# Optimization experiments

Measured on AMD Instinct MI355X. Metric: run time of the kernel, lower is better.

The kernel has to match this reference:

```python
import jax, jax.numpy as jnp
import numpy as np

N_NODES = 50000
N_EDGES = 1600000
HIDDEN = 1024
NUM_CLASSES = 64


def setup_inputs() -> dict:
    key = jax.random.key(0)
    k1, k2, k3 = jax.random.split(key, 3)
    x = jax.random.normal(k1, (N_NODES, HIDDEN), dtype=jnp.float32)
    edge_index = jax.random.randint(k2, (2, N_EDGES), 0, N_NODES, dtype=jnp.int64)
    # Glorot-style init for the GCNConv linear weight, zero bias (PyG defaults)
    W = jax.random.normal(k3, (HIDDEN, NUM_CLASSES), dtype=jnp.float32) / np.sqrt(HIDDEN)
    b = jnp.zeros((NUM_CLASSES,), dtype=jnp.float32)
    return {"x": x, "edge_index": edge_index, "W": W, "b": b}


def reference(x, edge_index, W, b):
    # GCNConv: add self-loops, symmetric deg^{-1/2} normalization,
    # linear transform, gather-scale-scatter aggregation, bias, then softmax.
    n = x.shape[0]
    loops = jnp.arange(n, dtype=edge_index.dtype)
    src = jnp.concatenate([edge_index[0], loops])  # [E+N]
    dst = jnp.concatenate([edge_index[1], loops])  # [E+N]

    ones = jnp.ones(dst.shape[0], dtype=x.dtype)
    deg = jax.ops.segment_sum(ones, dst, num_segments=n)  # in-degree incl. self-loop
    deg_inv_sqrt = jnp.where(deg > 0, jax.lax.rsqrt(deg), 0.0)
    norm = deg_inv_sqrt[src] * deg_inv_sqrt[dst]  # [E+N]

    h = x @ W  # [N, C] dense GEMM (transform before propagate)
    msgs = h[src] * norm[:, None]  # gather + scale
    out = jax.ops.segment_sum(msgs, dst, num_segments=n) + b  # scatter-add
    return jax.nn.softmax(out, axis=1)
```

## Files before the change

kernel.cpp:

```cpp
#include <hip/hip_runtime.h>
#include <hip/hip_bf16.h>
#include <hip/hip_fp16.h>
#include <math.h>

#define HIDDEN 1024
#define NCLS 64
#define NB2 784
#define BCAP2 2560
#define CHUNK 4096
#define SMEM_BYTES 33280

typedef __attribute__((ext_vector_type(8))) short short8;
typedef __attribute__((ext_vector_type(4))) float f32x4;
typedef __attribute__((ext_vector_type(8))) _Float16 half8;

__device__ __forceinline__ short f2bf(float f) {
    __hip_bfloat16 b = __float2bfloat16(f);
    return __builtin_bit_cast(short, b);
}
__device__ __forceinline__ float bf2f(short s) {
    unsigned u = ((unsigned)(unsigned short)s) << 16;
    return __builtin_bit_cast(float, u);
}

__device__ __forceinline__ void async_copy16(void* lds, const void* g) {
    __builtin_amdgcn_global_load_lds(
        (const __attribute__((address_space(1))) unsigned int*)g,
        (__attribute__((address_space(3))) unsigned int*)lds, 16, 0, 0);
}

__global__ void wprep_kernel(const float* __restrict__ W,
                             short* __restrict__ wt_hi, short* __restrict__ wt_lo) {
    int idx = blockIdx.x * 256 + threadIdx.x;
    int c = idx >> 10;
    int k = idx & 1023;
    float f = W[(size_t)k * NCLS + c];
    short hb = f2bf(f);
    wt_hi[idx] = hb;
    wt_lo[idx] = f2bf(f - bf2f(hb));
}

__device__ void bucket_body(char* smem, const int* __restrict__ ei,
                            unsigned* __restrict__ pairs2, int* __restrict__ bcnt2,
                            int E, int bid) {
    int* hist  = (int*)smem;
    int* offs  = hist + 1024;
    int* cur   = offs + 1024;
    int* gbase = cur + 1024;
    unsigned* stage = (unsigned*)(gbase + 1024);
    int* nz = (int*)(stage + CHUNK);
    int* wsum = nz + 1;

    const int tid = threadIdx.x;
    const int base = bid * CHUNK;
    const int cnt_c = min(CHUNK, E - base);

    if (tid == 0) *nz = 0;
    #pragma unroll
    for (int j = 0; j < 4; ++j) { hist[tid + 256 * j] = 0; cur[tid + 256 * j] = 0; }
    __syncthreads();

    int found = 0;
    for (int j = tid; j < 1024; j += 256) {
        int e = base + j;
        if (e < E) found |= (ei[2 * e + 1] != 0);
    }
    if (found) atomicOr(nz, 1);
    __syncthreads();
    const int is64 = (*nz == 0);

    unsigned pr[16];
    #pragma unroll
    for (int j = 0; j < 16; ++j) {
        int e = base + j * 256 + tid;
        unsigned p = 0xFFFFFFFFu;
        if (e < E) {
            int s = is64 ? ei[2 * e] : ei[e];
            int d = is64 ? ei[2 * (E + e)] : ei[E + e];
            p = (unsigned)s | ((unsigned)d << 16);
            atomicAdd(&hist[d >> 6], 1);
        }
        pr[j] = p;
    }
    __syncthreads();

    const int b0 = 4 * tid;
    int h0 = hist[b0], h1 = hist[b0 + 1], h2 = hist[b0 + 2], h3 = hist[b0 + 3];
    int S = h0 + h1 + h2 + h3;
    int incl = S;
    #pragma unroll
    for (int d = 1; d < 64; d <<= 1) {
        int t2 = __shfl_up(incl, d);
        if ((tid & 63) >= d) incl += t2;
    }
    if ((tid & 63) == 63) wsum[tid >> 6] = incl;
    __syncthreads();
    int pre = 0;
    #pragma unroll
    for (int w = 0; w < 4; ++w)
        if (w < (tid >> 6)) pre += wsum[w];
    int ex = pre + incl - S;
    offs[b0] = ex;
    offs[b0 + 1] = ex + h0;
    offs[b0 + 2] = ex + h0 + h1;
    offs[b0 + 3] = ex + h0 + h1 + h2;
    if (h0 > 0) gbase[b0] = atomicAdd(&bcnt2[b0], h0);
    if (h1 > 0) gbase[b0 + 1] = atomicAdd(&bcnt2[b0 + 1], h1);
    if (h2 > 0) gbase[b0 + 2] = atomicAdd(&bcnt2[b0 + 2], h2);
    if (h3 > 0) gbase[b0 + 3] = atomicAdd(&bcnt2[b0 + 3], h3);
    __syncthreads();

    #pragma unroll
    for (int j = 0; j < 16; ++j) {
        unsigned p = pr[j];
        if (p != 0xFFFFFFFFu) {
            int b = (int)(p >> 22);
            int pos = offs[b] + atomicAdd(&cur[b], 1);
            stage[pos] = p;
        }
    }
    __syncthreads();
    for (int i = tid; i < cnt_c; i += 256) {
        unsigned p = stage[i];
        int b = (int)(p >> 22);
        pairs2[(size_t)b * BCAP2 + gbase[b] + (i - offs[b])] = p;
    }
    __syncthreads();
}

__device__ void gemm_body(char* smem, const float* __restrict__ x,
                          const short* __restrict__ wt_hi, const short* __restrict__ wt_lo,
                          _Float16* __restrict__ h16, int M, int bid) {
    char* As = smem;
    char* Bh = smem + 16 * 1040;
    char* Bl = smem + 24 * 1040;

    const int tid = threadIdx.x;
    const int wave = tid >> 6;
    const int lane = tid & 63;
    const int l15 = lane & 15, l4 = lane >> 4;
    const int row0 = bid * 64;

    const float* agp[4];
    #pragma unroll
    for (int i = 0; i < 4; ++i) {
        int rg = row0 + (wave * 4 + i) * 4 + (lane >> 4);
        if (rg > M - 1) rg = M - 1;
        int g = (lane & 15) ^ (((lane >> 4) & 3) << 2);
        agp[i] = x + (size_t)rg * HIDDEN + g * 4;
    }
    const short* bhp[2];
    const short* blp[2];
    #pragma unroll
    for (int i = 0; i < 2; ++i) {
        int c = (wave * 2 + i) * 8 + (lane >> 3);
        int g = (lane & 7) ^ ((lane >> 3) & 7);
        bhp[i] = wt_hi + (size_t)c * HIDDEN + g * 8;
        blp[i] = wt_lo + (size_t)c * HIDDEN + g * 8;
    }

    f32x4 acc[4];
    #pragma unroll
    for (int nf = 0; nf < 4; ++nf) acc[nf] = (f32x4){0.f, 0.f, 0.f, 0.f};

    const int rt = wave * 16 + l15;
    const int r3 = rt & 3;
    char* arow = As + (rt >> 2) * 1040 + r3 * 256;

    for (int k0 = 0; k0 < HIDDEN; k0 += 64) {
        #pragma unroll
        for (int i = 0; i < 4; ++i)
            async_copy16(As + (wave * 4 + i) * 1040, agp[i] + k0);
        #pragma unroll
        for (int i = 0; i < 2; ++i) {
            async_copy16(Bh + (wave * 2 + i) * 1040, bhp[i] + k0);
            async_copy16(Bl + (wave * 2 + i) * 1040, blp[i] + k0);
        }
        __syncthreads();

        #pragma unroll
        for (int kk = 0; kk < 2; ++kk) {
            int js = (kk * 8 + l4 * 2) ^ (r3 << 2);
            f32x4 af0 = *reinterpret_cast<const f32x4*>(arow + js * 16);
            f32x4 af1 = *reinterpret_cast<const f32x4*>(arow + js * 16 + 16);
            short8 ah, al;
            #pragma unroll
            for (int j = 0; j < 4; ++j) {
                short hb = f2bf(af0[j]);
                ah[j] = hb;
                al[j] = f2bf(af0[j] - bf2f(hb));
                short hb2 = f2bf(af1[j]);
                ah[j + 4] = hb2;
                al[j + 4] = f2bf(af1[j] - bf2f(hb2));
            }
            #pragma unroll
            for (int nf = 0; nf < 4; ++nf) {
                int c = l15 + 16 * nf;
                int jb = (kk * 4 + l4) ^ (c & 7);
                size_t boff = (size_t)(c >> 3) * 1040 + (c & 7) * 128 + jb * 16;
                short8 bh = *reinterpret_cast<const short8*>(Bh + boff);
                short8 bl = *reinterpret_cast<const short8*>(Bl + boff);
                acc[nf] = __builtin_amdgcn_mfma_f32_16x16x32_bf16(ah, bh, acc[nf], 0, 0, 0);
                acc[nf] = __builtin_amdgcn_mfma_f32_16x16x32_bf16(al, bh, acc[nf], 0, 0, 0);
                acc[nf] = __builtin_amdgcn_mfma_f32_16x16x32_bf16(ah, bl, acc[nf], 0, 0, 0);
            }
        }
        __syncthreads();
    }

    #pragma unroll
    for (int j = 0; j < 4; ++j) {
        int r = row0 + wave * 16 + l4 * 4 + j;
        if (r < M) {
            #pragma unroll
            for (int nf = 0; nf < 4; ++nf) {
                h16[(size_t)r * NCLS + l15 + 16 * nf] = (_Float16)acc[nf][j];
            }
        }
    }
}

__global__ __launch_bounds__(256) void fat_kernel(const float* __restrict__ x,
                                                  const short* __restrict__ wt_hi,
                                                  const short* __restrict__ wt_lo,
                                                  _Float16* __restrict__ h16, int M,
                                                  const int* __restrict__ ei,
                                                  unsigned* __restrict__ pairs2,
                                                  int* __restrict__ bcnt2, int E,
                                                  int nBucketBlocks, int nTiles,
                                                  int* __restrict__ tile_ctr) {
    __shared__ __align__(16) char smem[SMEM_BYTES];
    __shared__ int s_tile;
    const int bid = blockIdx.x;
    if (bid < nBucketBlocks)
        bucket_body(smem, ei, pairs2, bcnt2, E, bid);
    for (;;) {
        if (threadIdx.x == 0) s_tile = atomicAdd(tile_ctr, 1);
        __syncthreads();
        int t = s_tile;
        if (t >= nTiles) break;
        gemm_body(smem, x, wt_hi, wt_lo, h16, M, t);
    }
}

__global__ __launch_bounds__(256) void degree_kernel(const unsigned* __restrict__ pairs2,
                                                     const int* __restrict__ bcnt2,
                                                     float* __restrict__ dis, int n) {
    __shared__ int hist[256];
    const int tid = threadIdx.x;
    hist[tid] = 0;
    __syncthreads();
    #pragma unroll
    for (int gg = 0; gg < 4; ++gg) {
        int g = blockIdx.x * 4 + gg;
        const int cb = bcnt2[g];
        const unsigned* bp = pairs2 + (size_t)g * BCAP2;
        for (int i = tid; i < cb; i += 256)
            atomicAdd(&hist[gg * 64 + ((bp[i] >> 16) & 63)], 1);
    }
    __syncthreads();
    int node = blockIdx.x * 256 + tid;
    if (node < n) dis[node] = rsqrtf((float)hist[tid] + 1.0f);
}

__global__ __launch_bounds__(256) void agg_kernel(const unsigned* __restrict__ pairs2,
                                                  const int* __restrict__ bcnt2,
                                                  const _Float16* __restrict__ h16,
                                                  const float* __restrict__ dis,
                                                  const float* __restrict__ bias,
                                                  float* __restrict__ out, int n) {
    __shared__ int hist[64];
    __shared__ int offs[64];
    __shared__ int cur[64];
    __shared__ unsigned short ssrc[BCAP2];
    __shared__ float swt[BCAP2];
    const int tid = threadIdx.x;
    const int grp = blockIdx.x;
    const int base_node = grp * 64;
    if (base_node >= n) return;
    if (tid < 64) { hist[tid] = 0; cur[tid] = 0; }
    __syncthreads();
    const int cb = bcnt2[grp];
    const unsigned* bp = pairs2 + (size_t)grp * BCAP2;
    for (int i = tid; i < cb; i += 256)
        atomicAdd(&hist[(bp[i] >> 16) & 63], 1);
    __syncthreads();
    if (tid == 0) {
        int r = 0;
        #pragma unroll
        for (int k = 0; k < 64; ++k) { offs[k] = r; r += hist[k]; }
    }
    __syncthreads();
    for (int i = tid; i < cb; i += 256) {
        unsigned p = bp[i];
        int ln = (p >> 16) & 63;
        int pos = offs[ln] + atomicAdd(&cur[ln], 1);
        int s = (int)(p & 0xFFFFu);
        ssrc[pos] = (unsigned short)s;
        swt[pos] = dis[s];
    }
    __syncthreads();

    const int wave = tid >> 6;
    const int lane = tid & 63;
    const int q = lane & 7;
    const int g = lane >> 3;
    float bv[8];
    #pragma unroll
    for (int c = 0; c < 8; ++c) bv[c] = bias[q * 8 + c];

    for (int t = 0; t < 16; ++t) {
        int ln = wave * 16 + t;
        int node = base_node + ln;
        if (node >= n) continue;
        int len = hist[ln];
        int e0 = offs[ln];
        float di = rsqrtf((float)len + 1.0f);

        half8 hs = *reinterpret_cast<const half8*>(h16 + (size_t)node * NCLS + q * 8);
        float selfw = (g == 0) ? di : 0.f;
        float a[8], a2[8];
        #pragma unroll
        for (int c = 0; c < 8; ++c) { a[c] = (float)hs[c] * selfw; a2[c] = 0.f; }

        for (int i = 0; i < len; i += 16) {
            int i1 = i + g;
            bool v1 = i1 < len;
            int s1 = v1 ? (int)ssrc[e0 + i1] : 0;
            float w1 = v1 ? swt[e0 + i1] : 0.f;
            half8 r1 = *reinterpret_cast<const half8*>(h16 + (size_t)s1 * NCLS + q * 8);
            if (i + 8 < len) {
                int i2 = i + 8 + g;
                bool v2 = i2 < len;
                int s2 = v2 ? (int)ssrc[e0 + i2] : 0;
                float w2 = v2 ? swt[e0 + i2] : 0.f;
                half8 r2 = *reinterpret_cast<const half8*>(h16 + (size_t)s2 * NCLS + q * 8);
                #pragma unroll
                for (int c = 0; c < 8; ++c) a2[c] += w2 * (float)r2[c];
            }
            #pragma unroll
            for (int c = 0; c < 8; ++c) a[c] += w1 * (float)r1[c];
        }
        #pragma unroll
        for (int c = 0; c < 8; ++c) {
            float s = a[c] + a2[c];
            s += __shfl_xor(s, 8);
            s += __shfl_xor(s, 16);
            s += __shfl_xor(s, 32);
            a[c] = s * di + bv[c];
        }
        float m = a[0];
        #pragma unroll
        for (int c = 1; c < 8; ++c) m = fmaxf(m, a[c]);
        #pragma unroll
        for (int d = 1; d < 8; d <<= 1) m = fmaxf(m, __shfl_xor(m, d));
        float ex[8], sum = 0.f;
        #pragma unroll
        for (int c = 0; c < 8; ++c) { ex[c] = __expf(a[c] - m); sum += ex[c]; }
        #pragma unroll
        for (int d = 1; d < 8; d <<= 1) sum += __shfl_xor(sum, d);
        float inv = 1.f / sum;
        if (g == 0) {
            f32x4 o0 = {ex[0] * inv, ex[1] * inv, ex[2] * inv, ex[3] * inv};
            f32x4 o1 = {ex[4] * inv, ex[5] * inv, ex[6] * inv, ex[7] * inv};
            *reinterpret_cast<f32x4*>(out + (size_t)node * NCLS + q * 8) = o0;
            *reinterpret_cast<f32x4*>(out + (size_t)node * NCLS + q * 8 + 4) = o1;
        }
    }
}

extern "C" void kernel_launch(void* const* d_in, const int* in_sizes, int n_in,
                              void* d_out, int out_size, void* d_ws, size_t ws_size,
                              hipStream_t stream) {
    const float* x    = (const float*)d_in[0];
    const int*   ei   = (const int*)d_in[1];
    const float* W    = (const float*)d_in[2];
    const float* bias = (const float*)d_in[3];
    float* out = (float*)d_out;

    const int n = in_sizes[0] / HIDDEN;
    const int E = in_sizes[1] / 2;

    char* ws = (char*)d_ws;
    size_t off = 0;
    auto alloc = [&](size_t bytes) -> void* {
        void* p = (void*)(ws + off);
        off = (off + bytes + 255) & ~((size_t)255);
        return p;
    };
    int*      bcnt2  = (int*)alloc((size_t)(NB2 + 1) * 4);
    unsigned* pairs2 = (unsigned*)alloc((size_t)NB2 * BCAP2 * 4);
    float*    dis    = (float*)alloc((size_t)n * 4);
    _Float16* h16    = (_Float16*)alloc((size_t)n * NCLS * 2);
    short*    wt_hi  = (short*)alloc((size_t)NCLS * HIDDEN * 2);
    short*    wt_lo  = (short*)alloc((size_t)NCLS * HIDDEN * 2);
    (void)ws_size;

    hipMemsetAsync(bcnt2, 0, (size_t)(NB2 + 1) * 4, stream);

    wprep_kernel<<<(NCLS * HIDDEN) / 256, 256, 0, stream>>>(W, wt_hi, wt_lo);

    const int nTiles = (n + 63) / 64;
    const int nBucketBlocks = (E + CHUNK - 1) / CHUNK;
    fat_kernel<<<1024, 256, 0, stream>>>(
        x, wt_hi, wt_lo, h16, n, ei, pairs2, bcnt2, E,
        nBucketBlocks, nTiles, bcnt2 + NB2);

    const int nGroups = (n + 63) / 64;
    degree_kernel<<<(nGroups + 3) / 4, 256, 0, stream>>>(pairs2, bcnt2, dis, n);
    agg_kernel<<<nGroups, 256, 0, stream>>>(pairs2, bcnt2, h16, dis, bias, out, n);
}
```

Before: 148.9 us.

## Double-buffer GEMM LDS tiles with async prefetch and halve fat kernel grid

After: 153.0 us. +2.8%, slower.

```diff
diff --git a/kernel.cpp b/kernel.cpp
--- a/kernel.cpp
+++ b/kernel.cpp
@@ -8,7 +8,8 @@
 #define NB2 784
 #define BCAP2 2560
 #define CHUNK 4096
-#define SMEM_BYTES 33280
+#define BUFB 33280
+#define SMEM_BYTES (2 * BUFB)
 
 typedef __attribute__((ext_vector_type(8))) short short8;
 typedef __attribute__((ext_vector_type(4))) float f32x4;
@@ -131,10 +132,6 @@
 __device__ void gemm_body(char* smem, const float* __restrict__ x,
                           const short* __restrict__ wt_hi, const short* __restrict__ wt_lo,
                           _Float16* __restrict__ h16, int M, int bid) {
-    char* As = smem;
-    char* Bh = smem + 16 * 1040;
-    char* Bl = smem + 24 * 1040;
-
     const int tid = threadIdx.x;
     const int wave = tid >> 6;
     const int lane = tid & 63;
@@ -165,9 +162,12 @@
 
     const int rt = wave * 16 + l15;
     const int r3 = rt & 3;
-    char* arow = As + (rt >> 2) * 1040 + r3 * 256;
-
-    for (int k0 = 0; k0 < HIDDEN; k0 += 64) {
+    const int aoff = (rt >> 2) * 1040 + r3 * 256;
+
+    auto stage = [&](char* buf, int k0) {
+        char* As = buf;
+        char* Bh = buf + 16 * 1040;
+        char* Bl = buf + 24 * 1040;
         #pragma unroll
         for (int i = 0; i < 4; ++i)
             async_copy16(As + (wave * 4 + i) * 1040, agp[i] + k0);
@@ -176,8 +176,12 @@
             async_copy16(Bh + (wave * 2 + i) * 1040, bhp[i] + k0);
             async_copy16(Bl + (wave * 2 + i) * 1040, blp[i] + k0);
         }
-        __syncthreads();
-
+    };
+
+    auto compute = [&](char* buf) {
+        char* arow = buf + aoff;
+        char* Bh = buf + 16 * 1040;
+        char* Bl = buf + 24 * 1040;
         #pragma unroll
         for (int kk = 0; kk < 2; ++kk) {
             int js = (kk * 8 + l4 * 2) ^ (r3 << 2);
@@ -205,7 +209,22 @@
                 acc[nf] = __builtin_amdgcn_mfma_f32_16x16x32_bf16(ah, bl, acc[nf], 0, 0, 0);
             }
         }
-        __syncthreads();
+    };
+
+    stage(smem, 0);
+    int cur = 0;
+    #pragma unroll 2
+    for (int t = 0; t < 16; ++t) {
+        char* bc = smem + cur * BUFB;
+        if (t < 15) {
+            stage(smem + (cur ^ 1) * BUFB, (t + 1) * 64);
+            asm volatile("s_waitcnt vmcnt(8)\n\ts_barrier" ::: "memory");
+        } else {
+            asm volatile("s_waitcnt vmcnt(0)\n\ts_barrier" ::: "memory");
+        }
+        compute(bc);
+        asm volatile("s_barrier" ::: "memory");
+        cur ^= 1;
     }
 
     #pragma unroll
@@ -240,6 +259,7 @@
         int t = s_tile;
         if (t >= nTiles) break;
         gemm_body(smem, x, wt_hi, wt_lo, h16, M, t);
+        __syncthreads();
     }
 }
 
@@ -402,7 +422,7 @@
 
     const int nTiles = (n + 63) / 64;
     const int nBucketBlocks = (E + CHUNK - 1) / CHUNK;
-    fat_kernel<<<1024, 256, 0, stream>>>(
+    fat_kernel<<<512, 256, 0, stream>>>(
         x, wt_hi, wt_lo, h16, n, ei, pairs2, bcnt2, E,
         nBucketBlocks, nTiles, bcnt2 + NB2);
 
```

## Split bucket and GEMM kernels; add 4-deep async LDS ring pipeline to GEMM

Applied to the files above, without the earlier changes.

New measurement: 176.8 us. 18.7% more time.

```diff
diff --git a/kernel.cpp b/kernel.cpp
--- a/kernel.cpp
+++ b/kernel.cpp
@@ -8,7 +8,10 @@
 #define NB2 784
 #define BCAP2 2560
 #define CHUNK 4096
-#define SMEM_BYTES 33280
+#define KSTEP 32
+#define NKS 32
+#define BUF 16384
+#define RING 4
 
 typedef __attribute__((ext_vector_type(8))) short short8;
 typedef __attribute__((ext_vector_type(4))) float f32x4;
@@ -40,9 +43,10 @@
     wt_lo[idx] = f2bf(f - bf2f(hb));
 }
 
-__device__ void bucket_body(char* smem, const int* __restrict__ ei,
-                            unsigned* __restrict__ pairs2, int* __restrict__ bcnt2,
-                            int E, int bid) {
+__global__ __launch_bounds__(256) void bucket_kernel(const int* __restrict__ ei,
+                                                     unsigned* __restrict__ pairs2,
+                                                     int* __restrict__ bcnt2, int E) {
+    __shared__ __align__(16) char smem[32800];
     int* hist  = (int*)smem;
     int* offs  = hist + 1024;
     int* cur   = offs + 1024;
@@ -52,7 +56,7 @@
     int* wsum = nz + 1;
 
     const int tid = threadIdx.x;
-    const int base = bid * CHUNK;
+    const int base = blockIdx.x * CHUNK;
     const int cnt_c = min(CHUNK, E - base);
 
     if (tid == 0) *nz = 0;
@@ -125,64 +129,64 @@
         int b = (int)(p >> 22);
         pairs2[(size_t)b * BCAP2 + gbase[b] + (i - offs[b])] = p;
     }
-    __syncthreads();
-}
-
-__device__ void gemm_body(char* smem, const float* __restrict__ x,
-                          const short* __restrict__ wt_hi, const short* __restrict__ wt_lo,
-                          _Float16* __restrict__ h16, int M, int bid) {
-    char* As = smem;
-    char* Bh = smem + 16 * 1040;
-    char* Bl = smem + 24 * 1040;
-
+}
+
+__global__ __launch_bounds__(256) void gemm_kernel(const float* __restrict__ x,
+                                                   const short* __restrict__ wt_hi,
+                                                   const short* __restrict__ wt_lo,
+                                                   _Float16* __restrict__ h16, int M,
+                                                   int nTiles, int* __restrict__ tile_ctr) {
+    __shared__ __align__(16) char smem[RING * BUF];
+    __shared__ int s_tile;
     const int tid = threadIdx.x;
     const int wave = tid >> 6;
     const int lane = tid & 63;
     const int l15 = lane & 15, l4 = lane >> 4;
-    const int row0 = bid * 64;
-
-    const float* agp[4];
-    #pragma unroll
-    for (int i = 0; i < 4; ++i) {
-        int rg = row0 + (wave * 4 + i) * 4 + (lane >> 4);
-        if (rg > M - 1) rg = M - 1;
-        int g = (lane & 15) ^ (((lane >> 4) & 3) << 2);
-        agp[i] = x + (size_t)rg * HIDDEN + g * 4;
-    }
-    const short* bhp[2];
-    const short* blp[2];
-    #pragma unroll
-    for (int i = 0; i < 2; ++i) {
-        int c = (wave * 2 + i) * 8 + (lane >> 3);
-        int g = (lane & 7) ^ ((lane >> 3) & 7);
-        bhp[i] = wt_hi + (size_t)c * HIDDEN + g * 8;
-        blp[i] = wt_lo + (size_t)c * HIDDEN + g * 8;
-    }
-
-    f32x4 acc[4];
-    #pragma unroll
-    for (int nf = 0; nf < 4; ++nf) acc[nf] = (f32x4){0.f, 0.f, 0.f, 0.f};
+
+    const int ar0 = wave * 16 + (lane >> 3);
+    const int ar1 = wave * 16 + 8 + (lane >> 3);
+    const int ag  = ((lane & 7) ^ ((lane >> 3) & 7)) * 4;
+    const int bcol = wave * 16 + (lane >> 2);
+    const int bg  = ((lane & 3) ^ ((lane >> 2) & 3)) * 8;
 
     const int rt = wave * 16 + l15;
-    const int r3 = rt & 3;
-    char* arow = As + (rt >> 2) * 1040 + r3 * 256;
-
-    for (int k0 = 0; k0 < HIDDEN; k0 += 64) {
-        #pragma unroll
-        for (int i = 0; i < 4; ++i)
-            async_copy16(As + (wave * 4 + i) * 1040, agp[i] + k0);
-        #pragma unroll
-        for (int i = 0; i < 2; ++i) {
-            async_copy16(Bh + (wave * 2 + i) * 1040, bhp[i] + k0);
-            async_copy16(Bl + (wave * 2 + i) * 1040, blp[i] + k0);
-        }
+
+    for (;;) {
         __syncthreads();
-
-        #pragma unroll
-        for (int kk = 0; kk < 2; ++kk) {
-            int js = (kk * 8 + l4 * 2) ^ (r3 << 2);
-            f32x4 af0 = *reinterpret_cast<const f32x4*>(arow + js * 16);
-            f32x4 af1 = *reinterpret_cast<const f32x4*>(arow + js * 16 + 16);
+        if (tid == 0) s_tile = atomicAdd(tile_ctr, 1);
+        __syncthreads();
+        const int t = s_tile;
+        if (t >= nTiles) break;
+        const int row0 = t * 64;
+
+        const float* ap0 = x + (size_t)min(row0 + ar0, M - 1) * HIDDEN + ag;
+        const float* ap1 = x + (size_t)min(row0 + ar1, M - 1) * HIDDEN + ag;
+        const short* bhp = wt_hi + (size_t)bcol * HIDDEN + bg;
+        const short* blp = wt_lo + (size_t)bcol * HIDDEN + bg;
+
+        auto stage = [&](int step) {
+            int k0 = min(step, NKS - 1) * KSTEP;
+            char* buf = smem + (step & (RING - 1)) * BUF;
+            async_copy16(buf + wave * 2048, ap0 + k0);
+            async_copy16(buf + wave * 2048 + 1024, ap1 + k0);
+            async_copy16(buf + 8192 + wave * 1024, bhp + k0);
+            async_copy16(buf + 12288 + wave * 1024, blp + k0);
+        };
+
+        f32x4 acc[4];
+        #pragma unroll
+        for (int nf = 0; nf < 4; ++nf) acc[nf] = (f32x4){0.f, 0.f, 0.f, 0.f};
+
+        stage(0); stage(1); stage(2);
+        for (int tt = 0; tt < NKS; ++tt) {
+            stage(tt + 3);
+            asm volatile("s_waitcnt vmcnt(12)\n\ts_barrier" ::: "memory");
+            char* buf = smem + (tt & (RING - 1)) * BUF;
+            const int abyte = rt * 128;
+            f32x4 af0 = *reinterpret_cast<const f32x4*>(
+                buf + abyte + (((l4 * 2) ^ (rt & 7)) * 16));
+            f32x4 af1 = *reinterpret_cast<const f32x4*>(
+                buf + abyte + (((l4 * 2 + 1) ^ (rt & 7)) * 16));
             short8 ah, al;
             #pragma unroll
             for (int j = 0; j < 4; ++j) {
@@ -196,50 +200,27 @@
             #pragma unroll
             for (int nf = 0; nf < 4; ++nf) {
                 int c = l15 + 16 * nf;
-                int jb = (kk * 4 + l4) ^ (c & 7);
-                size_t boff = (size_t)(c >> 3) * 1040 + (c & 7) * 128 + jb * 16;
-                short8 bh = *reinterpret_cast<const short8*>(Bh + boff);
-                short8 bl = *reinterpret_cast<const short8*>(Bl + boff);
+                int bo = 8192 + c * 64 + ((l4 ^ (c & 3)) * 16);
+                short8 bh = *reinterpret_cast<const short8*>(buf + bo);
+                short8 bl = *reinterpret_cast<const short8*>(buf + bo + 4096);
                 acc[nf] = __builtin_amdgcn_mfma_f32_16x16x32_bf16(ah, bh, acc[nf], 0, 0, 0);
                 acc[nf] = __builtin_amdgcn_mfma_f32_16x16x32_bf16(al, bh, acc[nf], 0, 0, 0);
                 acc[nf] = __builtin_amdgcn_mfma_f32_16x16x32_bf16(ah, bl, acc[nf], 0, 0, 0);
             }
-        }
-        __syncthreads();
-    }
-
-    #pragma unroll
-    for (int j = 0; j < 4; ++j) {
-        int r = row0 + wave * 16 + l4 * 4 + j;
-        if (r < M) {
-            #pragma unroll
-            for (int nf = 0; nf < 4; ++nf) {
-                h16[(size_t)r * NCLS + l15 + 16 * nf] = (_Float16)acc[nf][j];
+            asm volatile("s_barrier" ::: "memory");
+        }
+        asm volatile("s_waitcnt vmcnt(0)" ::: "memory");
+
+        #pragma unroll
+        for (int j = 0; j < 4; ++j) {
+            int r = row0 + wave * 16 + l4 * 4 + j;
+            if (r < M) {
+                #pragma unroll
+                for (int nf = 0; nf < 4; ++nf) {
+                    h16[(size_t)r * NCLS + l15 + 16 * nf] = (_Float16)acc[nf][j];
+                }
             }
         }
-    }
-}
-
-__global__ __launch_bounds__(256) void fat_kernel(const float* __restrict__ x,
-                                                  const short* __restrict__ wt_hi,
-                                                  const short* __restrict__ wt_lo,
-                                                  _Float16* __restrict__ h16, int M,
-                                                  const int* __restrict__ ei,
-                                                  unsigned* __restrict__ pairs2,
-                                                  int* __restrict__ bcnt2, int E,
-                                                  int nBucketBlocks, int nTiles,
-                                                  int* __restrict__ tile_ctr) {
-    __shared__ __align__(16) char smem[SMEM_BYTES];
-    __shared__ int s_tile;
-    const int bid = blockIdx.x;
-    if (bid < nBucketBlocks)
-        bucket_body(smem, ei, pairs2, bcnt2, E, bid);
-    for (;;) {
-        if (threadIdx.x == 0) s_tile = atomicAdd(tile_ctr, 1);
-        __syncthreads();
-        int t = s_tile;
-        if (t >= nTiles) break;
-        gemm_body(smem, x, wt_hi, wt_lo, h16, M, t);
     }
 }
 
@@ -400,11 +381,11 @@
 
     wprep_kernel<<<(NCLS * HIDDEN) / 256, 256, 0, stream>>>(W, wt_hi, wt_lo);
 
+    const int nBucketBlocks = (E + CHUNK - 1) / CHUNK;
+    bucket_kernel<<<nBucketBlocks, 256, 0, stream>>>(ei, pairs2, bcnt2, E);
+
     const int nTiles = (n + 63) / 64;
-    const int nBucketBlocks = (E + CHUNK - 1) / CHUNK;
-    fat_kernel<<<1024, 256, 0, stream>>>(
-        x, wt_hi, wt_lo, h16, n, ei, pairs2, bcnt2, E,
-        nBucketBlocks, nTiles, bcnt2 + NB2);
+    gemm_kernel<<<512, 256, 0, stream>>>(x, wt_hi, wt_lo, h16, n, nTiles, bcnt2 + NB2);
 
     const int nGroups = (n + 63) / 64;
     degree_kernel<<<(nGroups + 3) / 4, 256, 0, stream>>>(pairs2, bcnt2, dis, n);
```
